# Optimization experiments

Measured on AMD Instinct MI355X. Metric: run time of the kernel, lower is better.

## Reference

```python
import jax, jax.numpy as jnp
import numpy as np

EMB_DIM = 64
HIDDEN = 128
NUM_CLASSES = 2
N_NODES = 100000
N_EDGES = 1250000


def setup_inputs() -> dict:
    key = jax.random.key(0)
    k_h, k_e, k_w1, k_b1, k_w2, k_b2 = jax.random.split(key, 6)
    h = jax.random.normal(k_h, (N_NODES, EMB_DIM), dtype=jnp.float32)
    edge_index = jax.random.randint(k_e, (2, N_EDGES), 0, N_NODES, dtype=jnp.int64)
    # Linear params (torch Linear: y = x @ W.T + b); store as [in, out] for x @ W
    lim1 = 1.0 / np.sqrt(2 * EMB_DIM)
    W1 = jax.random.uniform(k_w1, (2 * EMB_DIM, HIDDEN), minval=-lim1, maxval=lim1, dtype=jnp.float32)
    b1 = jax.random.uniform(k_b1, (HIDDEN,), minval=-lim1, maxval=lim1, dtype=jnp.float32)
    lim2 = 1.0 / np.sqrt(HIDDEN)
    W2 = jax.random.uniform(k_w2, (HIDDEN, NUM_CLASSES), minval=-lim2, maxval=lim2, dtype=jnp.float32)
    b2 = jax.random.uniform(k_b2, (NUM_CLASSES,), minval=-lim2, maxval=lim2, dtype=jnp.float32)
    return {"h": h, "edge_index": edge_index, "W1": W1, "b1": b1, "W2": W2, "b2": b2}


def reference(h, edge_index, W1, b1, W2, b2):
    # Gather endpoint embeddings: [E, emb], concat -> [E, 2*emb]
    h_src = h[edge_index[0]]
    h_dst = h[edge_index[1]]
    x = jnp.concatenate([h_src, h_dst], axis=-1)
    hid = jax.nn.relu(x @ W1 + b1)  # [E, hidden]
    return hid @ W2 + b2            # [E, num_classes]
```

## Files before the change

kernel.cpp:

```cpp
#include <hip/hip_runtime.h>
#include <hip/hip_bf16.h>
#include <cstdint>


constexpr int EMB = 64;
constexpr int HID = 128;

typedef int   i32x4 __attribute__((ext_vector_type(4)));
typedef short s16x8 __attribute__((ext_vector_type(8)));
typedef float f32x4 __attribute__((ext_vector_type(4)));

__device__ __forceinline__ unsigned short f2bf(float x) {
    unsigned u = __float_as_uint(x);
    u = (u + 0x7fffu + ((u >> 16) & 1u)) >> 16;
    return (unsigned short)u;
}

__global__ void w1max_kernel(const float* __restrict__ W1, unsigned* __restrict__ swbits) {
    const int i = blockIdx.x * 256 + threadIdx.x;
    float4 v = *reinterpret_cast<const float4*>(W1 + (size_t)i * 4);
    float m = fmaxf(fmaxf(fabsf(v.x), fabsf(v.y)), fmaxf(fabsf(v.z), fabsf(v.w)));
    #pragma unroll
    for (int off = 1; off < 64; off <<= 1) m = fmaxf(m, __shfl_xor(m, off, 64));
    if ((threadIdx.x & 63) == 0) atomicMax(swbits, __float_as_uint(m));
}

__global__ void quant_h_fused(const float* __restrict__ h, float* __restrict__ sc,
                              char* __restrict__ hq, int total) {
    __shared__ float red[4];
    const int g = blockIdx.x, t = threadIdx.x;
    const size_t base = (size_t)g * 4096 + (size_t)t * 16;
    const bool full = (base < (size_t)total);
    float4 v[4];
    float m = 0.f;
    if (full) {
        #pragma unroll
        for (int q = 0; q < 4; ++q) {
            v[q] = *reinterpret_cast<const float4*>(h + base + q * 4);
            m = fmaxf(m, fmaxf(fmaxf(fabsf(v[q].x), fabsf(v[q].y)),
                               fmaxf(fabsf(v[q].z), fabsf(v[q].w))));
        }
    }
    #pragma unroll
    for (int off = 1; off < 64; off <<= 1) m = fmaxf(m, __shfl_xor(m, off, 64));
    if ((t & 63) == 0) red[t >> 6] = m;
    __syncthreads();
    const float gmax = fmaxf(fmaxf(red[0], red[1]), fmaxf(red[2], red[3]));
    const float scale = fmaxf(gmax / 127.f, 1e-20f);
    if (t == 0) sc[g] = scale;
    if (!full) return;
    const float inv = 1.0f / scale;
    unsigned w[4];
    #pragma unroll
    for (int q = 0; q < 4; ++q) {
        int a = max(-127, min(127, __float2int_rn(v[q].x * inv)));
        int b = max(-127, min(127, __float2int_rn(v[q].y * inv)));
        int c = max(-127, min(127, __float2int_rn(v[q].z * inv)));
        int d = max(-127, min(127, __float2int_rn(v[q].w * inv)));
        w[q] = (a & 255) | ((b & 255) << 8) | ((c & 255) << 16) | ((unsigned)(d & 255) << 24);
    }
    *reinterpret_cast<uint4*>(hq + base) = make_uint4(w[0], w[1], w[2], w[3]);
}

__global__ void pack_tabs_i8(const float* __restrict__ W1, const float* __restrict__ W2,
                             const float* __restrict__ swp,
                             char* __restrict__ w1q, unsigned short* __restrict__ w2t) {
    const int i = blockIdx.x * blockDim.x + threadIdx.x;
    if (i < 16384) {
        const int j = i & 15, lane = (i >> 4) & 63, half = (i >> 10) & 1, mt = i >> 11;
        const int k = half * 64 + (lane >> 4) * 16 + j;
        const int n = mt * 16 + (lane & 15);
        const float inv = 127.f / fmaxf(swp[0], 1e-18f);
        w1q[i] = (char)max(-127, min(127, __float2int_rn(W1[(size_t)k * HID + n] * inv)));
    } else if (i < 16384 + 2048) {
        const int q = i - 16384;
        const int j = q & 7, lane = (q >> 3) & 63, ks = q >> 9;
        const int tc = lane & 15, bq = lane >> 4;
        const int mt = ks * 2 + (j >> 2), r = j & 3;
        w2t[q] = (tc < 2) ? f2bf(W2[(mt * 16 + bq * 4 + r) * 2 + tc]) : (unsigned short)0;
    }
}

__global__ __launch_bounds__(256, 2)
void edge_mlp_i8v2(const char* __restrict__ hq,
                   const float* __restrict__ scg,
                   const float* __restrict__ swp,
                   const char* __restrict__ w1q,
                   const unsigned short* __restrict__ w2t,
                   const int* __restrict__ eidx,
                   const float* __restrict__ b1,
                   const float* __restrict__ b2,
                   float* __restrict__ out, int E, int nTiles, int nG64)
{
    __shared__ uint4 w1s[1024];
    __shared__ float sS[1600];
    __shared__ float b1s[128];
    {
        const uint4* src = reinterpret_cast<const uint4*>(w1q);
        #pragma unroll
        for (int r = 0; r < 4; ++r)
            w1s[r * 256 + threadIdx.x] = src[r * 256 + threadIdx.x];
        const float swv = swp[0] / 127.f;
        for (int i = threadIdx.x; i < nG64; i += 256) sS[i] = scg[i] * swv;
        if (threadIdx.x < 128) b1s[threadIdx.x] = b1[threadIdx.x];
    }
    __syncthreads();

    const int t = threadIdx.x, wid = t >> 6, lane = t & 63;
    const int tc = lane & 15, bq = lane >> 4;
    const i32x4* wq = reinterpret_cast<const i32x4*>(w1s) + lane;
    const float* b1v = b1s + bq * 4;

    s16x8 w2f[4];
    #pragma unroll
    for (int ks = 0; ks < 4; ++ks)
        w2f[ks] = *reinterpret_cast<const s16x8*>(w2t + (ks * 64 + lane) * 8);

    const float a20 = (bq == 0) ? b2[0] : 0.f;
    const float a21 = (bq == 0) ? b2[1] : 0.f;

    const int stride = gridDim.x * 4;
    int tile = blockIdx.x * 4 + wid;
    if (tile >= nTiles) return;

    auto LOADIDX = [&](int tl, int& s, int& d) {
        if (tl < nTiles) {
            const int e = min(tl * 16 + tc, E - 1);
            s = eidx[e]; d = eidx[E + e];
        } else { s = 0; d = 0; }
    };
    auto GATHER = [&](int s, int d, i32x4& xS, i32x4& xD, float& ssw, float& sdw) {
        xS = *reinterpret_cast<const i32x4*>(hq + (size_t)s * EMB + bq * 16);
        xD = *reinterpret_cast<const i32x4*>(hq + (size_t)d * EMB + bq * 16);
        ssw = sS[s >> 6];
        sdw = sS[d >> 6];
    };
    auto COMPUTE = [&](int tl, i32x4 xS, i32x4 xD, float ssw, float sdw) {
        const i32x4 z = {0, 0, 0, 0};
        f32x4 o = {a20, a21, 0.f, 0.f};
        #pragma unroll
        for (int ks2 = 0; ks2 < 4; ++ks2) {
            const int mt0 = ks2 * 2, mt1 = mt0 + 1;
            i32x4 aS0 = __builtin_amdgcn_mfma_i32_16x16x64_i8(wq[(mt0 * 2 + 0) * 64], xS, z, 0, 0, 0);
            i32x4 aD0 = __builtin_amdgcn_mfma_i32_16x16x64_i8(wq[(mt0 * 2 + 1) * 64], xD, z, 0, 0, 0);
            i32x4 aS1 = __builtin_amdgcn_mfma_i32_16x16x64_i8(wq[(mt1 * 2 + 0) * 64], xS, z, 0, 0, 0);
            i32x4 aD1 = __builtin_amdgcn_mfma_i32_16x16x64_i8(wq[(mt1 * 2 + 1) * 64], xD, z, 0, 0, 0);
            const f32x4 bb0 = *reinterpret_cast<const f32x4*>(b1v + mt0 * 16);
            const f32x4 bb1 = *reinterpret_cast<const f32x4*>(b1v + mt1 * 16);
            s16x8 p;
            #pragma unroll
            for (int jj = 0; jj < 4; ++jj) {
                const int r = (jj & 1) * 2;
                float h0, h1;
                if (jj < 2) {
                    h0 = fmaxf(fmaf((float)aS0[r],     ssw, fmaf((float)aD0[r],     sdw, bb0[r]    )), 0.f);
                    h1 = fmaxf(fmaf((float)aS0[r + 1], ssw, fmaf((float)aD0[r + 1], sdw, bb0[r + 1])), 0.f);
                } else {
                    h0 = fmaxf(fmaf((float)aS1[r],     ssw, fmaf((float)aD1[r],     sdw, bb1[r]    )), 0.f);
                    h1 = fmaxf(fmaf((float)aS1[r + 1], ssw, fmaf((float)aD1[r + 1], sdw, bb1[r + 1])), 0.f);
                }
                __hip_bfloat162 bb = __float22bfloat162_rn(make_float2(h0, h1));
                reinterpret_cast<unsigned*>(&p)[jj] = *reinterpret_cast<unsigned*>(&bb);
            }
            o = __builtin_amdgcn_mfma_f32_16x16x32_bf16(w2f[ks2], p, o, 0, 0, 0);
        }
        if (lane < 16) {
            const int eo = tl * 16 + lane;
            if (eo < E)
                *reinterpret_cast<float2*>(out + (size_t)eo * 2) = make_float2(o[0], o[1]);
        }
    };

    int s0, d0, s1, d1, s2, d2;
    i32x4 xS0, xD0, xS1, xD1, xS2, xD2;
    float w0s, w0d, w1sc, w1d, w2sc, w2d;

    LOADIDX(tile, s0, d0);
    GATHER(s0, d0, xS0, xD0, w0s, w0d);
    LOADIDX(tile + stride, s1, d1);
    GATHER(s1, d1, xS1, xD1, w1sc, w1d);
    LOADIDX(tile + 2 * stride, s2, d2);

    while (true) {
        GATHER(s2, d2, xS2, xD2, w2sc, w2d);
        LOADIDX(tile + 3 * stride, s0, d0);
        COMPUTE(tile, xS0, xD0, w0s, w0d);
        tile += stride;
        if (tile >= nTiles) break;

        GATHER(s0, d0, xS0, xD0, w0s, w0d);
        LOADIDX(tile + 3 * stride, s1, d1);
        COMPUTE(tile, xS1, xD1, w1sc, w1d);
        tile += stride;
        if (tile >= nTiles) break;

        GATHER(s1, d1, xS1, xD1, w1sc, w1d);
        LOADIDX(tile + 3 * stride, s2, d2);
        COMPUTE(tile, xS2, xD2, w2sc, w2d);
        tile += stride;
        if (tile >= nTiles) break;
    }
}

__global__ void edge_mlp_naive(const float* __restrict__ h, const int* __restrict__ eidx,
                               const float* __restrict__ W1, const float* __restrict__ b1,
                               const float* __restrict__ W2, const float* __restrict__ b2,
                               float* __restrict__ out, int E) {
    const int e = blockIdx.x * 256 + threadIdx.x;
    if (e >= E) return;
    const float* hs = h + (size_t)eidx[e] * EMB;
    const float* hd = h + (size_t)eidx[E + e] * EMB;
    float o0 = b2[0], o1 = b2[1];
    for (int j = 0; j < HID; ++j) {
        float a = b1[j];
        for (int k = 0; k < EMB; ++k)
            a += hs[k] * W1[(size_t)k * HID + j] + hd[k] * W1[(size_t)(k + EMB) * HID + j];
        a = fmaxf(a, 0.f);
        o0 = fmaf(a, W2[j * 2 + 0], o0);
        o1 = fmaf(a, W2[j * 2 + 1], o1);
    }
    out[(size_t)e * 2 + 0] = o0;
    out[(size_t)e * 2 + 1] = o1;
}

extern "C" void kernel_launch(void* const* d_in, const int* in_sizes, int n_in,
                              void* d_out, int out_size, void* d_ws, size_t ws_size,
                              hipStream_t stream)
{
    const float* h  = (const float*)d_in[0];
    const int*   ei = (const int*)d_in[1];
    const float* W1 = (const float*)d_in[2];
    const float* b1 = (const float*)d_in[3];
    const float* W2 = (const float*)d_in[4];
    const float* b2 = (const float*)d_in[5];
    float* out = (float*)d_out;

    const int nNodes = in_sizes[0] / EMB;
    const int E      = in_sizes[1] / 2;
    const int nTiles = (E + 15) / 16;
    const int nG64   = (nNodes + 63) >> 6;
    const int total  = nNodes * EMB;

    const size_t hq_off = 0;
    const size_t sc_off = (size_t)nNodes * EMB;
    const size_t sw_off = sc_off + (size_t)nG64 * 4;
    const size_t w1_off = (sw_off + 4 + 15) & ~(size_t)15;
    const size_t w2_off = w1_off + 16384;
    const size_t need   = w2_off + 2048 * 2;

    if (ws_size >= need && nG64 <= 1600) {
        char*  ws  = (char*)d_ws;
        char*  hq  = ws + hq_off;
        float* scg = (float*)(ws + sc_off);
        unsigned* swb = (unsigned*)(ws + sw_off);
        char*  w1q = ws + w1_off;
        unsigned short* w2t = (unsigned short*)(ws + w2_off);

        hipMemsetAsync(swb, 0, 4, stream);
        hipLaunchKernelGGL(w1max_kernel, dim3(16), dim3(256), 0, stream, W1, swb);
        hipLaunchKernelGGL(quant_h_fused, dim3(nG64), dim3(256), 0, stream,
                           h, scg, hq, total);
        hipLaunchKernelGGL(pack_tabs_i8, dim3(72), dim3(256), 0, stream,
                           W1, W2, (const float*)swb, w1q, w2t);
        hipLaunchKernelGGL(edge_mlp_i8v2, dim3(1024), dim3(256), 0, stream,
                           hq, scg, (const float*)swb, w1q, w2t, ei, b1, b2,
                           out, E, nTiles, nG64);
    } else {
        hipLaunchKernelGGL(edge_mlp_naive, dim3((E + 255) / 256), dim3(256), 0, stream,
                           h, ei, W1, b1, W2, b2, out, E);
    }
}
```

Baseline: 75.34 us.

## Raise edge-MLP occupancy by shrinking LDS and registers, fold weight scale upstream

The per-group h scale is multiplied by the W1 scale inside the quantization kernel, so the edge kernel no longer stages a 1600-entry scale table in LDS and instead reads the scale from global memory per gather. W2 fragments move from registers into shared memory, the software pipeline depth drops from three tiles in flight to two, launch bounds go from 2 to 8 blocks per CU, and the grid grows from 1024 to 1792 blocks. The aim is to hide gather latency through higher occupancy instead of deeper per-wave prefetching. In exchange, each wave has less prefetch in flight and the scale lookups become global loads.

```diff
diff --git a/kernel.cpp b/kernel.cpp
--- a/kernel.cpp
+++ b/kernel.cpp
@@ -25,8 +25,8 @@
     if ((threadIdx.x & 63) == 0) atomicMax(swbits, __float_as_uint(m));
 }
 
-__global__ void quant_h_fused(const float* __restrict__ h, float* __restrict__ sc,
-                              char* __restrict__ hq, int total) {
+__global__ void quant_h_fused(const float* __restrict__ h, const unsigned* __restrict__ swb,
+                              float* __restrict__ scf, char* __restrict__ hq, int total) {
     __shared__ float red[4];
     const int g = blockIdx.x, t = threadIdx.x;
     const size_t base = (size_t)g * 4096 + (size_t)t * 16;
@@ -47,7 +47,10 @@
     __syncthreads();
     const float gmax = fmaxf(fmaxf(red[0], red[1]), fmaxf(red[2], red[3]));
     const float scale = fmaxf(gmax / 127.f, 1e-20f);
-    if (t == 0) sc[g] = scale;
+    if (t == 0) {
+        const float swv = __uint_as_float(swb[0]) / 127.f;
+        scf[g] = scale * swv;
+    }
     if (!full) return;
     const float inv = 1.0f / scale;
     unsigned w[4];
@@ -63,14 +66,14 @@
 }
 
 __global__ void pack_tabs_i8(const float* __restrict__ W1, const float* __restrict__ W2,
-                             const float* __restrict__ swp,
+                             const unsigned* __restrict__ swb,
                              char* __restrict__ w1q, unsigned short* __restrict__ w2t) {
     const int i = blockIdx.x * blockDim.x + threadIdx.x;
     if (i < 16384) {
         const int j = i & 15, lane = (i >> 4) & 63, half = (i >> 10) & 1, mt = i >> 11;
         const int k = half * 64 + (lane >> 4) * 16 + j;
         const int n = mt * 16 + (lane & 15);
-        const float inv = 127.f / fmaxf(swp[0], 1e-18f);
+        const float inv = 127.f / fmaxf(__uint_as_float(swb[0]), 1e-18f);
         w1q[i] = (char)max(-127, min(127, __float2int_rn(W1[(size_t)k * HID + n] * inv)));
     } else if (i < 16384 + 2048) {
         const int q = i - 16384;
@@ -81,40 +84,34 @@
     }
 }
 
-__global__ __launch_bounds__(256, 2)
-void edge_mlp_i8v2(const char* __restrict__ hq,
-                   const float* __restrict__ scg,
-                   const float* __restrict__ swp,
+__global__ __launch_bounds__(256, 8)
+void edge_mlp_i8v3(const char* __restrict__ hq,
+                   const float* __restrict__ scf,
                    const char* __restrict__ w1q,
                    const unsigned short* __restrict__ w2t,
                    const int* __restrict__ eidx,
                    const float* __restrict__ b1,
                    const float* __restrict__ b2,
-                   float* __restrict__ out, int E, int nTiles, int nG64)
+                   float* __restrict__ out, int E, int nTiles)
 {
     __shared__ uint4 w1s[1024];
-    __shared__ float sS[1600];
+    __shared__ uint4 w2s[256];
     __shared__ float b1s[128];
     {
         const uint4* src = reinterpret_cast<const uint4*>(w1q);
         #pragma unroll
         for (int r = 0; r < 4; ++r)
             w1s[r * 256 + threadIdx.x] = src[r * 256 + threadIdx.x];
-        const float swv = swp[0] / 127.f;
-        for (int i = threadIdx.x; i < nG64; i += 256) sS[i] = scg[i] * swv;
+        w2s[threadIdx.x] = *(reinterpret_cast<const uint4*>(w2t) + threadIdx.x);
         if (threadIdx.x < 128) b1s[threadIdx.x] = b1[threadIdx.x];
     }
     __syncthreads();
 
     const int t = threadIdx.x, wid = t >> 6, lane = t & 63;
     const int tc = lane & 15, bq = lane >> 4;
-    const i32x4* wq = reinterpret_cast<const i32x4*>(w1s) + lane;
+    const i32x4* wq  = reinterpret_cast<const i32x4*>(w1s) + lane;
+    const s16x8* wf2 = reinterpret_cast<const s16x8*>(w2s) + lane;
     const float* b1v = b1s + bq * 4;
-
-    s16x8 w2f[4];
-    #pragma unroll
-    for (int ks = 0; ks < 4; ++ks)
-        w2f[ks] = *reinterpret_cast<const s16x8*>(w2t + (ks * 64 + lane) * 8);
 
     const float a20 = (bq == 0) ? b2[0] : 0.f;
     const float a21 = (bq == 0) ? b2[1] : 0.f;
@@ -132,37 +129,31 @@
     auto GATHER = [&](int s, int d, i32x4& xS, i32x4& xD, float& ssw, float& sdw) {
         xS = *reinterpret_cast<const i32x4*>(hq + (size_t)s * EMB + bq * 16);
         xD = *reinterpret_cast<const i32x4*>(hq + (size_t)d * EMB + bq * 16);
-        ssw = sS[s >> 6];
-        sdw = sS[d >> 6];
+        ssw = scf[s >> 6];
+        sdw = scf[d >> 6];
     };
     auto COMPUTE = [&](int tl, i32x4 xS, i32x4 xD, float ssw, float sdw) {
         const i32x4 z = {0, 0, 0, 0};
         f32x4 o = {a20, a21, 0.f, 0.f};
         #pragma unroll
         for (int ks2 = 0; ks2 < 4; ++ks2) {
-            const int mt0 = ks2 * 2, mt1 = mt0 + 1;
-            i32x4 aS0 = __builtin_amdgcn_mfma_i32_16x16x64_i8(wq[(mt0 * 2 + 0) * 64], xS, z, 0, 0, 0);
-            i32x4 aD0 = __builtin_amdgcn_mfma_i32_16x16x64_i8(wq[(mt0 * 2 + 1) * 64], xD, z, 0, 0, 0);
-            i32x4 aS1 = __builtin_amdgcn_mfma_i32_16x16x64_i8(wq[(mt1 * 2 + 0) * 64], xS, z, 0, 0, 0);
-            i32x4 aD1 = __builtin_amdgcn_mfma_i32_16x16x64_i8(wq[(mt1 * 2 + 1) * 64], xD, z, 0, 0, 0);
-            const f32x4 bb0 = *reinterpret_cast<const f32x4*>(b1v + mt0 * 16);
-            const f32x4 bb1 = *reinterpret_cast<const f32x4*>(b1v + mt1 * 16);
             s16x8 p;
             #pragma unroll
-            for (int jj = 0; jj < 4; ++jj) {
-                const int r = (jj & 1) * 2;
-                float h0, h1;
-                if (jj < 2) {
-                    h0 = fmaxf(fmaf((float)aS0[r],     ssw, fmaf((float)aD0[r],     sdw, bb0[r]    )), 0.f);
-                    h1 = fmaxf(fmaf((float)aS0[r + 1], ssw, fmaf((float)aD0[r + 1], sdw, bb0[r + 1])), 0.f);
-                } else {
-                    h0 = fmaxf(fmaf((float)aS1[r],     ssw, fmaf((float)aD1[r],     sdw, bb1[r]    )), 0.f);
-                    h1 = fmaxf(fmaf((float)aS1[r + 1], ssw, fmaf((float)aD1[r + 1], sdw, bb1[r + 1])), 0.f);
+            for (int half = 0; half < 2; ++half) {
+                const int mt = ks2 * 2 + half;
+                i32x4 aS = __builtin_amdgcn_mfma_i32_16x16x64_i8(wq[(mt * 2 + 0) * 64], xS, z, 0, 0, 0);
+                i32x4 aD = __builtin_amdgcn_mfma_i32_16x16x64_i8(wq[(mt * 2 + 1) * 64], xD, z, 0, 0, 0);
+                const f32x4 bb = *reinterpret_cast<const f32x4*>(b1v + mt * 16);
+                #pragma unroll
+                for (int pr = 0; pr < 2; ++pr) {
+                    const int r = pr * 2;
+                    float h0 = fmaxf(fmaf((float)aS[r],     ssw, fmaf((float)aD[r],     sdw, bb[r]    )), 0.f);
+                    float h1 = fmaxf(fmaf((float)aS[r + 1], ssw, fmaf((float)aD[r + 1], sdw, bb[r + 1])), 0.f);
+                    __hip_bfloat162 bpk = __float22bfloat162_rn(make_float2(h0, h1));
+                    reinterpret_cast<unsigned*>(&p)[half * 2 + pr] = *reinterpret_cast<unsigned*>(&bpk);
                 }
-                __hip_bfloat162 bb = __float22bfloat162_rn(make_float2(h0, h1));
-                reinterpret_cast<unsigned*>(&p)[jj] = *reinterpret_cast<unsigned*>(&bb);
             }
-            o = __builtin_amdgcn_mfma_f32_16x16x32_bf16(w2f[ks2], p, o, 0, 0, 0);
+            o = __builtin_amdgcn_mfma_f32_16x16x32_bf16(wf2[ks2 * 64], p, o, 0, 0, 0);
         }
         if (lane < 16) {
             const int eo = tl * 16 + lane;
@@ -171,32 +162,24 @@
         }
     };
 
-    int s0, d0, s1, d1, s2, d2;
-    i32x4 xS0, xD0, xS1, xD1, xS2, xD2;
-    float w0s, w0d, w1sc, w1d, w2sc, w2d;
+    int s0, d0, s1, d1;
+    i32x4 xS0, xD0, xS1, xD1;
+    float a0s, a0d, a1s, a1d;
 
     LOADIDX(tile, s0, d0);
-    GATHER(s0, d0, xS0, xD0, w0s, w0d);
+    GATHER(s0, d0, xS0, xD0, a0s, a0d);
     LOADIDX(tile + stride, s1, d1);
-    GATHER(s1, d1, xS1, xD1, w1sc, w1d);
-    LOADIDX(tile + 2 * stride, s2, d2);
 
     while (true) {
-        GATHER(s2, d2, xS2, xD2, w2sc, w2d);
-        LOADIDX(tile + 3 * stride, s0, d0);
-        COMPUTE(tile, xS0, xD0, w0s, w0d);
+        GATHER(s1, d1, xS1, xD1, a1s, a1d);
+        LOADIDX(tile + 2 * stride, s0, d0);
+        COMPUTE(tile, xS0, xD0, a0s, a0d);
         tile += stride;
         if (tile >= nTiles) break;
 
-        GATHER(s0, d0, xS0, xD0, w0s, w0d);
-        LOADIDX(tile + 3 * stride, s1, d1);
-        COMPUTE(tile, xS1, xD1, w1sc, w1d);
-        tile += stride;
-        if (tile >= nTiles) break;
-
-        GATHER(s1, d1, xS1, xD1, w1sc, w1d);
-        LOADIDX(tile + 3 * stride, s2, d2);
-        COMPUTE(tile, xS2, xD2, w2sc, w2d);
+        GATHER(s0, d0, xS0, xD0, a0s, a0d);
+        LOADIDX(tile + 2 * stride, s1, d1);
+        COMPUTE(tile, xS1, xD1, a1s, a1d);
         tile += stride;
         if (tile >= nTiles) break;
     }
@@ -248,10 +231,10 @@
     const size_t w2_off = w1_off + 16384;
     const size_t need   = w2_off + 2048 * 2;
 
-    if (ws_size >= need && nG64 <= 1600) {
+    if (ws_size >= need) {
         char*  ws  = (char*)d_ws;
         char*  hq  = ws + hq_off;
-        float* scg = (float*)(ws + sc_off);
+        float* scf = (float*)(ws + sc_off);
         unsigned* swb = (unsigned*)(ws + sw_off);
         char*  w1q = ws + w1_off;
         unsigned short* w2t = (unsigned short*)(ws + w2_off);
@@ -259,12 +242,11 @@
         hipMemsetAsync(swb, 0, 4, stream);
         hipLaunchKernelGGL(w1max_kernel, dim3(16), dim3(256), 0, stream, W1, swb);
         hipLaunchKernelGGL(quant_h_fused, dim3(nG64), dim3(256), 0, stream,
-                           h, scg, hq, total);
+                           h, swb, scf, hq, total);
         hipLaunchKernelGGL(pack_tabs_i8, dim3(72), dim3(256), 0, stream,
-                           W1, W2, (const float*)swb, w1q, w2t);
-        hipLaunchKernelGGL(edge_mlp_i8v2, dim3(1024), dim3(256), 0, stream,
-                           hq, scg, (const float*)swb, w1q, w2t, ei, b1, b2,
-                           out, E, nTiles, nG64);
+                           W1, W2, swb, w1q, w2t);
+        hipLaunchKernelGGL(edge_mlp_i8v3, dim3(1792), dim3(256), 0, stream,
+                           hq, scf, w1q, w2t, ei, b1, b2, out, E, nTiles);
     } else {
         hipLaunchKernelGGL(edge_mlp_naive, dim3((E + 255) / 256), dim3(256), 0, stream,
                            h, ei, W1, b1, W2, b2, out, E);
```

Measured after the change: 79.65 us. 1.06x slower.
